# Kernel tuning notes

Hardware: AMD Instinct MI355X
Metric: run time of the kernel (lower is better)

## Reference

```python
import jax, jax.numpy as jnp
import numpy as np

N_NODES = 100000
N_EDGES = 3200000
C_FEAT = 512
F_OUT = 1


def setup_inputs() -> dict:
    key = jax.random.key(0)
    k1, k2, k3 = jax.random.split(key, 3)
    x = jax.random.normal(k1, (N_NODES, C_FEAT), dtype=jnp.float32)
    edge_index = jax.random.randint(k2, (2, N_EDGES), 0, N_NODES, dtype=jnp.int64)
    # GCNConv lin weight (glorot-ish scale) and zero-init bias, as in PyG defaults
    W = jax.random.normal(k3, (F_OUT, C_FEAT), dtype=jnp.float32) / np.sqrt(C_FEAT)
    b = jnp.zeros((F_OUT,), dtype=jnp.float32)
    return {"x": x, "edge_index": edge_index, "W": W, "b": b}


def reference(x, edge_index, W, b):
    N = x.shape[0]
    # GCNConv: project first (lin has no bias), then normalized aggregation
    h = x @ W.T  # [N, F_OUT]
    # add self-loops
    loops = jnp.arange(N, dtype=edge_index.dtype)
    row = jnp.concatenate([edge_index[0], loops])  # source
    col = jnp.concatenate([edge_index[1], loops])  # target
    # symmetric normalization: deg over targets (incl. self-loop weight 1)
    deg = jax.ops.segment_sum(jnp.ones_like(col, dtype=h.dtype), col, num_segments=N)
    dinv = jnp.where(deg > 0, jax.lax.rsqrt(deg), 0.0)
    norm = dinv[row] * dinv[col]  # [E+N]
    msg = h[row] * norm[:, None]  # gather + scale
    out = jax.ops.segment_sum(msg, col, num_segments=N) + b  # scatter-add + bias
    # F_out == 1 branch of forward
    return jax.nn.sigmoid(out)
```

## Files before the change

### kernel.cpp

```cpp
#include <hip/hip_runtime.h>
#include <hip/hip_fp16.h>
#include <math.h>

#define NN 100000
#define NE 3200000
#define CF 512

#define NPARTS  8
#define PART    12500
#define NSLICES 64
#define EPB     (NE / NSLICES)
#define NPB     (NSLICES * NPARTS)

#define OFF_H    12800000
#define OFF_G    13200000
#define OFF_DINV 13600000

__device__ __forceinline__ bool detect_f64(const int* __restrict__ e32) {
    unsigned v = ((const unsigned*)e32)[2 * (threadIdx.x & 63) + 1];
    return __ballot(v != 0u) == 0ULL;
}

__device__ __forceinline__ int4 load_col4(const int* __restrict__ e32, bool f64, int e) {
    if (f64) {
        const int4* q = (const int4*)(e32 + 2 * (NE + e));
        int4 a = q[0], b = q[1];
        return make_int4(a.x, a.z, b.x, b.z);
    }
    return *(const int4*)(e32 + NE + e);
}

__device__ __forceinline__ int4 load_row4(const int* __restrict__ e32, bool f64, int e) {
    if (f64) {
        const int4* q = (const int4*)(e32 + 2 * e);
        int4 a = q[0], b = q[1];
        return make_int4(a.x, a.z, b.x, b.z);
    }
    return *(const int4*)(e32 + e);
}

#define NODES_PER_BLK 196

__global__ __launch_bounds__(1024) void deg_h_kernel(const int* __restrict__ e32,
                                                     const float* __restrict__ x,
                                                     const float* __restrict__ W,
                                                     unsigned short* __restrict__ deg_part,
                                                     float* __restrict__ h) {
    __shared__ int hist[PART];
    int tid = threadIdx.x;
    for (int i = tid; i < PART; i += 1024) hist[i] = 0;
    __syncthreads();

    int w = tid >> 6, lane = tid & 63;
    if (w < 12) {
        bool f64 = detect_f64(e32);
        int p = blockIdx.x >> 6;
        int s = blockIdx.x & 63;
        int lo = p * PART;
        int base = s * EPB;
        for (int e = base + tid * 4; e < base + EPB; e += 3072) {
            int4 c = load_col4(e32, f64, e);
            unsigned l0 = (unsigned)(c.x - lo), l1 = (unsigned)(c.y - lo);
            unsigned l2 = (unsigned)(c.z - lo), l3 = (unsigned)(c.w - lo);
            if (l0 < PART) atomicAdd(&hist[l0], 1);
            if (l1 < PART) atomicAdd(&hist[l1], 1);
            if (l2 < PART) atomicAdd(&hist[l2], 1);
            if (l3 < PART) atomicAdd(&hist[l3], 1);
        }
    } else {
        const float4* Wr = (const float4*)W;
        float4 w0 = Wr[lane], w1 = Wr[lane + 64];
        int start = blockIdx.x * NODES_PER_BLK;
        int end = start + NODES_PER_BLK;
        for (int i = start + (w - 12) * 2; i < end; i += 8) {
            int i1 = i + 1;
            float s0 = 0.f, s1 = 0.f;
            if (i < NN) {
                const float4* xr = (const float4*)(x + (size_t)i * CF);
                float4 a = xr[lane], bq = xr[lane + 64];
                s0 = a.x * w0.x + a.y * w0.y + a.z * w0.z + a.w * w0.w
                   + bq.x * w1.x + bq.y * w1.y + bq.z * w1.z + bq.w * w1.w;
            }
            if (i1 < NN) {
                const float4* xr = (const float4*)(x + (size_t)i1 * CF);
                float4 a = xr[lane], bq = xr[lane + 64];
                s1 = a.x * w0.x + a.y * w0.y + a.z * w0.z + a.w * w0.w
                   + bq.x * w1.x + bq.y * w1.y + bq.z * w1.z + bq.w * w1.w;
            }
#pragma unroll
            for (int off = 32; off >= 1; off >>= 1) {
                s0 += __shfl_down(s0, off, 64);
                s1 += __shfl_down(s1, off, 64);
            }
            if (lane == 0) {
                if (i < NN) h[i] = s0;
                if (i1 < NN) h[i1] = s1;
            }
        }
    }
    __syncthreads();
    unsigned short* outp = deg_part + (size_t)blockIdx.x * PART;
    for (int i = tid; i < PART; i += 1024) outp[i] = (unsigned short)hist[i];
}

__global__ void dinv_g_kernel(const unsigned short* __restrict__ deg_part,
                              const float* __restrict__ h,
                              float* __restrict__ dinv,
                              float* __restrict__ g) {
    int i = blockIdx.x * blockDim.x + threadIdx.x;
    if (i >= NN) return;
    int p = i / PART, l = i - p * PART;
    const unsigned short* bp = deg_part + ((size_t)(p << 6)) * PART + l;
    int d = 1;
#pragma unroll
    for (int s = 0; s < NSLICES; ++s) d += bp[(size_t)s * PART];
    float di = rsqrtf((float)d);
    dinv[i] = di;
    g[i] = h[i] * di;
}

__global__ __launch_bounds__(1024) void scatter_lds_kernel(const int* __restrict__ e32,
                                                           const float* __restrict__ g,
                                                           __half* __restrict__ s_part) {
    __shared__ float hs[PART];
    int tid = threadIdx.x;
    for (int i = tid; i < PART; i += 1024) hs[i] = 0.f;
    __syncthreads();

    bool f64 = detect_f64(e32);
    int p = blockIdx.x >> 6;
    int s = blockIdx.x & 63;
    int lo = p * PART;
    int base = s * EPB;
    for (int e = base + tid * 4; e < base + EPB; e += 4096) {
        int4 c = load_col4(e32, f64, e);
        int4 r = load_row4(e32, f64, e);
        unsigned l0 = (unsigned)(c.x - lo), l1 = (unsigned)(c.y - lo);
        unsigned l2 = (unsigned)(c.z - lo), l3 = (unsigned)(c.w - lo);
        if (l0 < PART) atomicAdd(&hs[l0], g[r.x]);
        if (l1 < PART) atomicAdd(&hs[l1], g[r.y]);
        if (l2 < PART) atomicAdd(&hs[l2], g[r.z]);
        if (l3 < PART) atomicAdd(&hs[l3], g[r.w]);
    }
    __syncthreads();
    __half* outp = s_part + (size_t)blockIdx.x * PART;
    for (int i = tid; i < PART; i += 1024) outp[i] = __float2half(hs[i]);
}

__global__ void final_kernel(const __half* __restrict__ s_part,
                             const float* __restrict__ g,
                             const float* __restrict__ dinv,
                             const float* __restrict__ b,
                             float* __restrict__ out) {
    int i = blockIdx.x * blockDim.x + threadIdx.x;
    if (i >= NN) return;
    int p = i / PART, l = i - p * PART;
    const __half* bp = s_part + ((size_t)(p << 6)) * PART + l;
    float acc = g[i];
#pragma unroll
    for (int s = 0; s < NSLICES; ++s) acc += __half2float(bp[(size_t)s * PART]);
    float v = dinv[i] * acc + b[0];
    out[i] = 1.f / (1.f + expf(-v));
}

extern "C" void kernel_launch(void* const* d_in, const int* in_sizes, int n_in,
                              void* d_out, int out_size, void* d_ws, size_t ws_size,
                              hipStream_t stream) {
    const float* x = (const float*)d_in[0];
    const int* eidx = (const int*)d_in[1];
    const float* W = (const float*)d_in[2];
    const float* b = (const float*)d_in[3];
    float* out = (float*)d_out;

    char* ws = (char*)d_ws;
    unsigned short* part_u16 = (unsigned short*)(ws);
    __half* part_h = (__half*)(ws);
    float* h = (float*)(ws + OFF_H);
    float* g = (float*)(ws + OFF_G);
    float* dinv = (float*)(ws + OFF_DINV);

    deg_h_kernel<<<NPB, 1024, 0, stream>>>(eidx, x, W, part_u16, h);
    dinv_g_kernel<<<(NN + 255) / 256, 256, 0, stream>>>(part_u16, h, dinv, g);
    scatter_lds_kernel<<<NPB, 1024, 0, stream>>>(eidx, g, part_h);
    final_kernel<<<(NN + 255) / 256, 256, 0, stream>>>(part_h, g, dinv, b, out);
}
```

Before: 368.4 us.

## Replace partitioned LDS histograms with direct global atomics for degree and scatter

The per-partition shared-memory histograms with fp16/u16 partial buffers are dropped in favour of direct global atomicAdd into a single float sum array and a single uint degree array, cleared by a memset. This removes the 8x redundant edge scans, the partial-buffer writes and the 64-way reductions in the finalisation kernels. In exchange it relies on global atomic throughput and contention in L2 on MI355X, and the float atomic ordering becomes nondeterministic. The degree/projection kernel is also split into separate edge and projection blocks of 256 threads.

```diff
diff --git a/kernel.cpp b/kernel.cpp
--- a/kernel.cpp
+++ b/kernel.cpp
@@ -1,27 +1,22 @@
 #include <hip/hip_runtime.h>
-#include <hip/hip_fp16.h>
 #include <math.h>
 
 #define NN 100000
 #define NE 3200000
 #define CF 512
 
-#define NPARTS  8
-#define PART    12500
-#define NSLICES 64
-#define EPB     (NE / NSLICES)
-#define NPB     (NSLICES * NPARTS)
+#define OFF_S    0
+#define OFF_DEG  400000
+#define OFF_H    800000
+#define OFF_G    1200000
+#define OFF_DINV 1600000
 
-#define OFF_H    12800000
-#define OFF_G    13200000
-#define OFF_DINV 13600000
-
-__device__ __forceinline__ bool detect_f64(const int* __restrict__ e32) {
+__device__ __forceinline__ bool detect_f64(const int* e32) {
     unsigned v = ((const unsigned*)e32)[2 * (threadIdx.x & 63) + 1];
     return __ballot(v != 0u) == 0ULL;
 }
 
-__device__ __forceinline__ int4 load_col4(const int* __restrict__ e32, bool f64, int e) {
+__device__ __forceinline__ int4 load_col4(const int* e32, bool f64, int e) {
     if (f64) {
         const int4* q = (const int4*)(e32 + 2 * (NE + e));
         int4 a = q[0], b = q[1];
@@ -29,8 +24,7 @@
     }
     return *(const int4*)(e32 + NE + e);
 }
-
-__device__ __forceinline__ int4 load_row4(const int* __restrict__ e32, bool f64, int e) {
+__device__ __forceinline__ int4 load_row4(const int* e32, bool f64, int e) {
     if (f64) {
         const int4* q = (const int4*)(e32 + 2 * e);
         int4 a = q[0], b = q[1];
@@ -39,43 +33,37 @@
     return *(const int4*)(e32 + e);
 }
 
-#define NODES_PER_BLK 196
+#define EDGE_BLKS 512
+#define H_BLKS    1536
+#define K1_BLKS   (EDGE_BLKS + H_BLKS)
 
-__global__ __launch_bounds__(1024) void deg_h_kernel(const int* __restrict__ e32,
-                                                     const float* __restrict__ x,
-                                                     const float* __restrict__ W,
-                                                     unsigned short* __restrict__ deg_part,
-                                                     float* __restrict__ h) {
-    __shared__ int hist[PART];
-    int tid = threadIdx.x;
-    for (int i = tid; i < PART; i += 1024) hist[i] = 0;
-    __syncthreads();
-
-    int w = tid >> 6, lane = tid & 63;
-    if (w < 12) {
+__global__ __launch_bounds__(256) void deg_h_kernel(const int* __restrict__ e32,
+                                                    const float* __restrict__ x,
+                                                    const float* __restrict__ W,
+                                                    unsigned* __restrict__ deg,
+                                                    float* __restrict__ h) {
+    int blk = blockIdx.x;
+    if (blk < EDGE_BLKS) {
         bool f64 = detect_f64(e32);
-        int p = blockIdx.x >> 6;
-        int s = blockIdx.x & 63;
-        int lo = p * PART;
-        int base = s * EPB;
-        for (int e = base + tid * 4; e < base + EPB; e += 3072) {
+        int gid = blk * 256 + threadIdx.x;
+        const int STRIDE = EDGE_BLKS * 256 * 4;
+        for (int e = gid * 4; e < NE; e += STRIDE) {
             int4 c = load_col4(e32, f64, e);
-            unsigned l0 = (unsigned)(c.x - lo), l1 = (unsigned)(c.y - lo);
-            unsigned l2 = (unsigned)(c.z - lo), l3 = (unsigned)(c.w - lo);
-            if (l0 < PART) atomicAdd(&hist[l0], 1);
-            if (l1 < PART) atomicAdd(&hist[l1], 1);
-            if (l2 < PART) atomicAdd(&hist[l2], 1);
-            if (l3 < PART) atomicAdd(&hist[l3], 1);
+            atomicAdd(&deg[c.x], 1u);
+            atomicAdd(&deg[c.y], 1u);
+            atomicAdd(&deg[c.z], 1u);
+            atomicAdd(&deg[c.w], 1u);
         }
     } else {
+        int wave = (blk - EDGE_BLKS) * 4 + (threadIdx.x >> 6);
+        int lane = threadIdx.x & 63;
         const float4* Wr = (const float4*)W;
         float4 w0 = Wr[lane], w1 = Wr[lane + 64];
-        int start = blockIdx.x * NODES_PER_BLK;
-        int end = start + NODES_PER_BLK;
-        for (int i = start + (w - 12) * 2; i < end; i += 8) {
+        const int NWAVES = H_BLKS * 4;
+        for (int i = wave * 2; i < NN; i += NWAVES * 2) {
             int i1 = i + 1;
             float s0 = 0.f, s1 = 0.f;
-            if (i < NN) {
+            {
                 const float4* xr = (const float4*)(x + (size_t)i * CF);
                 float4 a = xr[lane], bq = xr[lane + 64];
                 s0 = a.x * w0.x + a.y * w0.y + a.z * w0.z + a.w * w0.w
@@ -93,73 +81,50 @@
                 s1 += __shfl_down(s1, off, 64);
             }
             if (lane == 0) {
-                if (i < NN) h[i] = s0;
+                h[i] = s0;
                 if (i1 < NN) h[i1] = s1;
             }
         }
     }
-    __syncthreads();
-    unsigned short* outp = deg_part + (size_t)blockIdx.x * PART;
-    for (int i = tid; i < PART; i += 1024) outp[i] = (unsigned short)hist[i];
 }
 
-__global__ void dinv_g_kernel(const unsigned short* __restrict__ deg_part,
-                              const float* __restrict__ h,
-                              float* __restrict__ dinv,
-                              float* __restrict__ g) {
-    int i = blockIdx.x * blockDim.x + threadIdx.x;
+__global__ __launch_bounds__(256) void dinv_g_kernel(const unsigned* __restrict__ deg,
+                                                     const float* __restrict__ h,
+                                                     float* __restrict__ dinv,
+                                                     float* __restrict__ g) {
+    int i = blockIdx.x * 256 + threadIdx.x;
     if (i >= NN) return;
-    int p = i / PART, l = i - p * PART;
-    const unsigned short* bp = deg_part + ((size_t)(p << 6)) * PART + l;
-    int d = 1;
-#pragma unroll
-    for (int s = 0; s < NSLICES; ++s) d += bp[(size_t)s * PART];
-    float di = rsqrtf((float)d);
+    float di = rsqrtf((float)(1u + deg[i]));
     dinv[i] = di;
     g[i] = h[i] * di;
 }
 
-__global__ __launch_bounds__(1024) void scatter_lds_kernel(const int* __restrict__ e32,
-                                                           const float* __restrict__ g,
-                                                           __half* __restrict__ s_part) {
-    __shared__ float hs[PART];
-    int tid = threadIdx.x;
-    for (int i = tid; i < PART; i += 1024) hs[i] = 0.f;
-    __syncthreads();
-
+#define SC_BLKS 1024
+__global__ __launch_bounds__(256) void scatter_kernel(const int* __restrict__ e32,
+                                                      const float* __restrict__ g,
+                                                      float* __restrict__ s) {
     bool f64 = detect_f64(e32);
-    int p = blockIdx.x >> 6;
-    int s = blockIdx.x & 63;
-    int lo = p * PART;
-    int base = s * EPB;
-    for (int e = base + tid * 4; e < base + EPB; e += 4096) {
+    int gid = blockIdx.x * 256 + threadIdx.x;
+    const int STRIDE = SC_BLKS * 256 * 4;
+    for (int e = gid * 4; e < NE; e += STRIDE) {
         int4 c = load_col4(e32, f64, e);
         int4 r = load_row4(e32, f64, e);
-        unsigned l0 = (unsigned)(c.x - lo), l1 = (unsigned)(c.y - lo);
-        unsigned l2 = (unsigned)(c.z - lo), l3 = (unsigned)(c.w - lo);
-        if (l0 < PART) atomicAdd(&hs[l0], g[r.x]);
-        if (l1 < PART) atomicAdd(&hs[l1], g[r.y]);
-        if (l2 < PART) atomicAdd(&hs[l2], g[r.z]);
-        if (l3 < PART) atomicAdd(&hs[l3], g[r.w]);
+        float g0 = g[r.x], g1 = g[r.y], g2 = g[r.z], g3 = g[r.w];
+        atomicAdd(&s[c.x], g0);
+        atomicAdd(&s[c.y], g1);
+        atomicAdd(&s[c.z], g2);
+        atomicAdd(&s[c.w], g3);
     }
-    __syncthreads();
-    __half* outp = s_part + (size_t)blockIdx.x * PART;
-    for (int i = tid; i < PART; i += 1024) outp[i] = __float2half(hs[i]);
 }
 
-__global__ void final_kernel(const __half* __restrict__ s_part,
-                             const float* __restrict__ g,
-                             const float* __restrict__ dinv,
-                             const float* __restrict__ b,
-                             float* __restrict__ out) {
-    int i = blockIdx.x * blockDim.x + threadIdx.x;
+__global__ __launch_bounds__(256) void final_kernel(const float* __restrict__ s,
+                                                    const float* __restrict__ g,
+                                                    const float* __restrict__ dinv,
+                                                    const float* __restrict__ b,
+                                                    float* __restrict__ out) {
+    int i = blockIdx.x * 256 + threadIdx.x;
     if (i >= NN) return;
-    int p = i / PART, l = i - p * PART;
-    const __half* bp = s_part + ((size_t)(p << 6)) * PART + l;
-    float acc = g[i];
-#pragma unroll
-    for (int s = 0; s < NSLICES; ++s) acc += __half2float(bp[(size_t)s * PART]);
-    float v = dinv[i] * acc + b[0];
+    float v = dinv[i] * (s[i] + g[i]) + b[0];
     out[i] = 1.f / (1.f + expf(-v));
 }
 
@@ -173,14 +138,16 @@
     float* out = (float*)d_out;
 
     char* ws = (char*)d_ws;
-    unsigned short* part_u16 = (unsigned short*)(ws);
-    __half* part_h = (__half*)(ws);
+    float* s = (float*)(ws + OFF_S);
+    unsigned* deg = (unsigned*)(ws + OFF_DEG);
     float* h = (float*)(ws + OFF_H);
     float* g = (float*)(ws + OFF_G);
     float* dinv = (float*)(ws + OFF_DINV);
 
-    deg_h_kernel<<<NPB, 1024, 0, stream>>>(eidx, x, W, part_u16, h);
-    dinv_g_kernel<<<(NN + 255) / 256, 256, 0, stream>>>(part_u16, h, dinv, g);
-    scatter_lds_kernel<<<NPB, 1024, 0, stream>>>(eidx, g, part_h);
-    final_kernel<<<(NN + 255) / 256, 256, 0, stream>>>(part_h, g, dinv, b, out);
+    hipMemsetAsync(ws, 0, 800000, stream);
+
+    deg_h_kernel<<<K1_BLKS, 256, 0, stream>>>(eidx, x, W, deg, h);
+    dinv_g_kernel<<<(NN + 255) / 256, 256, 0, stream>>>(deg, h, dinv, g);
+    scatter_kernel<<<SC_BLKS, 256, 0, stream>>>(eidx, g, s);
+    final_kernel<<<(NN + 255) / 256, 256, 0, stream>>>(s, g, dinv, b, out);
 }
```

After: 574.2 us. 55.8% more time.

## Fuse GCN pipeline into single cooperative kernel with grid syncs

Applied to the files above, without the earlier changes.

Replaces the four-kernel sequence (degree histogram plus projection, dinv/g, LDS scatter, final reduce) with one cooperative kernel. It uses grid.sync between phases and keeps h and dinv in LDS instead of global memory. The goal is to remove inter-kernel launch gaps and some global round trips. The trade-off is the cost of grid-wide barriers and a required co-residency of all 512 1024-thread blocks. If the cooperative launch fails, it falls back to the old kernels.

```diff
diff --git a/kernel.cpp b/kernel.cpp
--- a/kernel.cpp
+++ b/kernel.cpp
@@ -1,6 +1,9 @@
 #include <hip/hip_runtime.h>
 #include <hip/hip_fp16.h>
+#include <hip/hip_cooperative_groups.h>
 #include <math.h>
+
+namespace cg = cooperative_groups;
 
 #define NN 100000
 #define NE 3200000
@@ -11,17 +14,18 @@
 #define NSLICES 64
 #define EPB     (NE / NSLICES)
 #define NPB     (NSLICES * NPARTS)
-
-#define OFF_H    12800000
-#define OFF_G    13200000
+#define NODES_PER_BLK 196
+
+#define OFF_G    12800000
+#define OFF_H    13200000
 #define OFF_DINV 13600000
 
-__device__ __forceinline__ bool detect_f64(const int* __restrict__ e32) {
+__device__ __forceinline__ bool detect_f64(const int* e32) {
     unsigned v = ((const unsigned*)e32)[2 * (threadIdx.x & 63) + 1];
     return __ballot(v != 0u) == 0ULL;
 }
 
-__device__ __forceinline__ int4 load_col4(const int* __restrict__ e32, bool f64, int e) {
+__device__ __forceinline__ int4 load_col4(const int* e32, bool f64, int e) {
     if (f64) {
         const int4* q = (const int4*)(e32 + 2 * (NE + e));
         int4 a = q[0], b = q[1];
@@ -29,8 +33,7 @@
     }
     return *(const int4*)(e32 + NE + e);
 }
-
-__device__ __forceinline__ int4 load_row4(const int* __restrict__ e32, bool f64, int e) {
+__device__ __forceinline__ int4 load_row4(const int* e32, bool f64, int e) {
     if (f64) {
         const int4* q = (const int4*)(e32 + 2 * e);
         int4 a = q[0], b = q[1];
@@ -39,7 +42,119 @@
     return *(const int4*)(e32 + e);
 }
 
-#define NODES_PER_BLK 196
+__global__ __launch_bounds__(1024, 8) void gcn_fused(const int* e32, const float* x,
+                                                     const float* W, const float* bias,
+                                                     unsigned short* part_u16,
+                                                     __half* part_h,
+                                                     float* g, float* out) {
+    __shared__ int hist[PART];
+    __shared__ float h_lds[NODES_PER_BLK];
+    __shared__ float dinv_lds[NODES_PER_BLK];
+    cg::grid_group grid = cg::this_grid();
+
+    int tid = threadIdx.x;
+    int blk = blockIdx.x;
+    int w = tid >> 6, lane = tid & 63;
+    bool f64 = detect_f64(e32);
+    int p = blk >> 6, s = blk & 63;
+    int lo = p * PART, base = s * EPB;
+
+    for (int i = tid; i < PART; i += 1024) hist[i] = 0;
+    __syncthreads();
+    if (w < 12) {
+        for (int e = base + tid * 4; e < base + EPB; e += 3072) {
+            int4 c = load_col4(e32, f64, e);
+            unsigned l0 = (unsigned)(c.x - lo), l1 = (unsigned)(c.y - lo);
+            unsigned l2 = (unsigned)(c.z - lo), l3 = (unsigned)(c.w - lo);
+            if (l0 < PART) atomicAdd(&hist[l0], 1);
+            if (l1 < PART) atomicAdd(&hist[l1], 1);
+            if (l2 < PART) atomicAdd(&hist[l2], 1);
+            if (l3 < PART) atomicAdd(&hist[l3], 1);
+        }
+    } else {
+        const float4* Wr = (const float4*)W;
+        float4 w0 = Wr[lane], w1 = Wr[lane + 64];
+        int start = blk * NODES_PER_BLK;
+        int end = start + NODES_PER_BLK;
+        for (int i = start + (w - 12) * 2; i < end; i += 8) {
+            int i1 = i + 1;
+            float s0 = 0.f, s1 = 0.f;
+            if (i < NN) {
+                const float4* xr = (const float4*)(x + (size_t)i * CF);
+                float4 a = xr[lane], bq = xr[lane + 64];
+                s0 = a.x * w0.x + a.y * w0.y + a.z * w0.z + a.w * w0.w
+                   + bq.x * w1.x + bq.y * w1.y + bq.z * w1.z + bq.w * w1.w;
+            }
+            if (i1 < NN) {
+                const float4* xr = (const float4*)(x + (size_t)i1 * CF);
+                float4 a = xr[lane], bq = xr[lane + 64];
+                s1 = a.x * w0.x + a.y * w0.y + a.z * w0.z + a.w * w0.w
+                   + bq.x * w1.x + bq.y * w1.y + bq.z * w1.z + bq.w * w1.w;
+            }
+#pragma unroll
+            for (int off = 32; off >= 1; off >>= 1) {
+                s0 += __shfl_down(s0, off, 64);
+                s1 += __shfl_down(s1, off, 64);
+            }
+            if (lane == 0) {
+                h_lds[i - start] = s0;
+                h_lds[i1 - start] = s1;
+            }
+        }
+    }
+    __syncthreads();
+    {
+        unsigned short* outp = part_u16 + (size_t)blk * PART;
+        for (int i = tid; i < PART; i += 1024) outp[i] = (unsigned short)hist[i];
+    }
+    __threadfence();
+    grid.sync();
+
+    int node = blk * NODES_PER_BLK + tid;
+    if (tid < NODES_PER_BLK && node < NN) {
+        int pp = node / PART, l = node - pp * PART;
+        const unsigned short* bp = part_u16 + ((size_t)(pp << 6)) * PART + l;
+        int d = 1;
+#pragma unroll 16
+        for (int ss = 0; ss < NSLICES; ++ss) d += bp[(size_t)ss * PART];
+        float di = rsqrtf((float)d);
+        dinv_lds[tid] = di;
+        g[node] = h_lds[tid] * di;
+    }
+    __threadfence();
+    grid.sync();
+
+    float* histf = (float*)hist;
+    for (int i = tid; i < PART; i += 1024) histf[i] = 0.f;
+    __syncthreads();
+    for (int e = base + tid * 4; e < base + EPB; e += 4096) {
+        int4 c = load_col4(e32, f64, e);
+        int4 r = load_row4(e32, f64, e);
+        unsigned l0 = (unsigned)(c.x - lo), l1 = (unsigned)(c.y - lo);
+        unsigned l2 = (unsigned)(c.z - lo), l3 = (unsigned)(c.w - lo);
+        if (l0 < PART) atomicAdd(&histf[l0], g[r.x]);
+        if (l1 < PART) atomicAdd(&histf[l1], g[r.y]);
+        if (l2 < PART) atomicAdd(&histf[l2], g[r.z]);
+        if (l3 < PART) atomicAdd(&histf[l3], g[r.w]);
+    }
+    __syncthreads();
+    {
+        __half* outp = part_h + (size_t)blk * PART;
+        for (int i = tid; i < PART; i += 1024) outp[i] = __float2half(histf[i]);
+    }
+    __threadfence();
+    grid.sync();
+
+    if (tid < NODES_PER_BLK && node < NN) {
+        int pp = node / PART, l = node - pp * PART;
+        const __half* bp = part_h + ((size_t)(pp << 6)) * PART + l;
+        float acc = g[node];
+#pragma unroll 16
+        for (int ss = 0; ss < NSLICES; ++ss) acc += __half2float(bp[(size_t)ss * PART]);
+        float v = dinv_lds[tid] * acc + bias[0];
+        out[node] = 1.f / (1.f + expf(-v));
+    }
+}
 
 __global__ __launch_bounds__(1024) void deg_h_kernel(const int* __restrict__ e32,
                                                      const float* __restrict__ x,
@@ -50,7 +165,6 @@
     int tid = threadIdx.x;
     for (int i = tid; i < PART; i += 1024) hist[i] = 0;
     __syncthreads();
-
     int w = tid >> 6, lane = tid & 63;
     if (w < 12) {
         bool f64 = detect_f64(e32);
@@ -126,7 +240,6 @@
     int tid = threadIdx.x;
     for (int i = tid; i < PART; i += 1024) hs[i] = 0.f;
     __syncthreads();
-
     bool f64 = detect_f64(e32);
     int p = blockIdx.x >> 6;
     int s = blockIdx.x & 63;
@@ -175,12 +288,19 @@
     char* ws = (char*)d_ws;
     unsigned short* part_u16 = (unsigned short*)(ws);
     __half* part_h = (__half*)(ws);
+    float* g = (float*)(ws + OFF_G);
     float* h = (float*)(ws + OFF_H);
-    float* g = (float*)(ws + OFF_G);
     float* dinv = (float*)(ws + OFF_DINV);
 
-    deg_h_kernel<<<NPB, 1024, 0, stream>>>(eidx, x, W, part_u16, h);
-    dinv_g_kernel<<<(NN + 255) / 256, 256, 0, stream>>>(part_u16, h, dinv, g);
-    scatter_lds_kernel<<<NPB, 1024, 0, stream>>>(eidx, g, part_h);
-    final_kernel<<<(NN + 255) / 256, 256, 0, stream>>>(part_h, g, dinv, b, out);
-}
+    void* kargs[] = {(void*)&eidx, (void*)&x, (void*)&W, (void*)&b,
+                     (void*)&part_u16, (void*)&part_h, (void*)&g, (void*)&out};
+    hipError_t err = hipLaunchCooperativeKernel((const void*)gcn_fused,
+                                                dim3(NPB), dim3(1024),
+                                                kargs, 0, stream);
+    if (err != hipSuccess) {
+        deg_h_kernel<<<NPB, 1024, 0, stream>>>(eidx, x, W, part_u16, h);
+        dinv_g_kernel<<<(NN + 255) / 256, 256, 0, stream>>>(part_u16, h, dinv, g);
+        scatter_lds_kernel<<<NPB, 1024, 0, stream>>>(eidx, g, part_h);
+        final_kernel<<<(NN + 255) / 256, 256, 0, stream>>>(part_h, g, dinv, b, out);
+    }
+}
```

Result: slower. 1.117 ms (+203.1%).

## Fuse final reduction into scatter kernel via last-block counter, halve slices

Applied to the files above, without the earlier changes.

Merges the final per-node reduction and sigmoid into the scatter kernel: each partition's last-arriving block, found through an atomic counter, sums the fp16 partials and writes the output. It also halves the number of edge slices per partition to 32, giving 256 blocks instead of 512, so there are fewer partials to reduce. The gathers of g are hoisted ahead of the LDS atomics so the loads can overlap. The aim is to drop one kernel launch and cut partial-sum traffic, at the cost of fewer blocks to fill the GPU and a serial tail in one block per partition.

```diff
diff --git a/kernel.cpp b/kernel.cpp
--- a/kernel.cpp
+++ b/kernel.cpp
@@ -11,17 +11,24 @@
 #define NSLICES 64
 #define EPB     (NE / NSLICES)
 #define NPB     (NSLICES * NPARTS)
-
-#define OFF_H    12800000
-#define OFF_G    13200000
-#define OFF_DINV 13600000
-
-__device__ __forceinline__ bool detect_f64(const int* __restrict__ e32) {
+#define NODES_PER_BLK 196
+
+#define SNSL    32
+#define SEPB    (NE / SNSL)
+#define SNPB    (SNSL * NPARTS)
+
+#define OFF_SPART 12800000
+#define OFF_G     19200000
+#define OFF_H     19600000
+#define OFF_DINV  20000000
+#define OFF_CTR   20400000
+
+__device__ __forceinline__ bool detect_f64(const int* e32) {
     unsigned v = ((const unsigned*)e32)[2 * (threadIdx.x & 63) + 1];
     return __ballot(v != 0u) == 0ULL;
 }
 
-__device__ __forceinline__ int4 load_col4(const int* __restrict__ e32, bool f64, int e) {
+__device__ __forceinline__ int4 load_col4(const int* e32, bool f64, int e) {
     if (f64) {
         const int4* q = (const int4*)(e32 + 2 * (NE + e));
         int4 a = q[0], b = q[1];
@@ -29,8 +36,7 @@
     }
     return *(const int4*)(e32 + NE + e);
 }
-
-__device__ __forceinline__ int4 load_row4(const int* __restrict__ e32, bool f64, int e) {
+__device__ __forceinline__ int4 load_row4(const int* e32, bool f64, int e) {
     if (f64) {
         const int4* q = (const int4*)(e32 + 2 * e);
         int4 a = q[0], b = q[1];
@@ -39,18 +45,17 @@
     return *(const int4*)(e32 + e);
 }
 
-#define NODES_PER_BLK 196
-
 __global__ __launch_bounds__(1024) void deg_h_kernel(const int* __restrict__ e32,
                                                      const float* __restrict__ x,
                                                      const float* __restrict__ W,
                                                      unsigned short* __restrict__ deg_part,
-                                                     float* __restrict__ h) {
+                                                     float* __restrict__ h,
+                                                     unsigned* __restrict__ ctr) {
     __shared__ int hist[PART];
     int tid = threadIdx.x;
+    if (blockIdx.x == 0 && tid < 8) ctr[tid] = 0u;
     for (int i = tid; i < PART; i += 1024) hist[i] = 0;
     __syncthreads();
-
     int w = tid >> 6, lane = tid & 63;
     if (w < 12) {
         bool f64 = detect_f64(e32);
@@ -119,48 +124,61 @@
     g[i] = h[i] * di;
 }
 
-__global__ __launch_bounds__(1024) void scatter_lds_kernel(const int* __restrict__ e32,
-                                                           const float* __restrict__ g,
-                                                           __half* __restrict__ s_part) {
+__global__ __launch_bounds__(1024) void scatter_final(const int* __restrict__ e32,
+                                                      const float* __restrict__ g,
+                                                      const float* __restrict__ dinv,
+                                                      const float* __restrict__ b,
+                                                      __half* __restrict__ spart,
+                                                      unsigned* __restrict__ ctr,
+                                                      float* __restrict__ out) {
     __shared__ float hs[PART];
+    __shared__ int lastflag;
     int tid = threadIdx.x;
     for (int i = tid; i < PART; i += 1024) hs[i] = 0.f;
     __syncthreads();
 
     bool f64 = detect_f64(e32);
-    int p = blockIdx.x >> 6;
-    int s = blockIdx.x & 63;
+    int p = blockIdx.x >> 5;
+    int s = blockIdx.x & 31;
     int lo = p * PART;
-    int base = s * EPB;
-    for (int e = base + tid * 4; e < base + EPB; e += 4096) {
+    int base = s * SEPB;
+    for (int e = base + tid * 4; e < base + SEPB; e += 4096) {
         int4 c = load_col4(e32, f64, e);
         int4 r = load_row4(e32, f64, e);
+        float g0 = g[r.x], g1 = g[r.y], g2 = g[r.z], g3 = g[r.w];
         unsigned l0 = (unsigned)(c.x - lo), l1 = (unsigned)(c.y - lo);
         unsigned l2 = (unsigned)(c.z - lo), l3 = (unsigned)(c.w - lo);
-        if (l0 < PART) atomicAdd(&hs[l0], g[r.x]);
-        if (l1 < PART) atomicAdd(&hs[l1], g[r.y]);
-        if (l2 < PART) atomicAdd(&hs[l2], g[r.z]);
-        if (l3 < PART) atomicAdd(&hs[l3], g[r.w]);
-    }
-    __syncthreads();
-    __half* outp = s_part + (size_t)blockIdx.x * PART;
-    for (int i = tid; i < PART; i += 1024) outp[i] = __float2half(hs[i]);
-}
-
-__global__ void final_kernel(const __half* __restrict__ s_part,
-                             const float* __restrict__ g,
-                             const float* __restrict__ dinv,
-                             const float* __restrict__ b,
-                             float* __restrict__ out) {
-    int i = blockIdx.x * blockDim.x + threadIdx.x;
-    if (i >= NN) return;
-    int p = i / PART, l = i - p * PART;
-    const __half* bp = s_part + ((size_t)(p << 6)) * PART + l;
-    float acc = g[i];
-#pragma unroll
-    for (int s = 0; s < NSLICES; ++s) acc += __half2float(bp[(size_t)s * PART]);
-    float v = dinv[i] * acc + b[0];
-    out[i] = 1.f / (1.f + expf(-v));
+        if (l0 < PART) atomicAdd(&hs[l0], g0);
+        if (l1 < PART) atomicAdd(&hs[l1], g1);
+        if (l2 < PART) atomicAdd(&hs[l2], g2);
+        if (l3 < PART) atomicAdd(&hs[l3], g3);
+    }
+    __syncthreads();
+    {
+        __half* outp = spart + (size_t)blockIdx.x * PART;
+        for (int i = tid; i < PART; i += 1024) outp[i] = __float2half(hs[i]);
+    }
+
+    __threadfence();
+    __syncthreads();
+    if (tid == 0) {
+        unsigned old = atomicAdd(&ctr[p], 1u);
+        lastflag = (old == (unsigned)(SNSL - 1)) ? 1 : 0;
+    }
+    __syncthreads();
+    if (!lastflag) return;
+    __threadfence();
+
+    const __half* bp = spart + (size_t)(p * SNSL) * PART;
+    float bias = b[0];
+    for (int l = tid; l < PART; l += 1024) {
+        float acc = 0.f;
+#pragma unroll 8
+        for (int s2 = 0; s2 < SNSL; ++s2) acc += __half2float(bp[(size_t)s2 * PART + l]);
+        int i = lo + l;
+        float v = dinv[i] * (acc + g[i]) + bias;
+        out[i] = 1.f / (1.f + expf(-v));
+    }
 }
 
 extern "C" void kernel_launch(void* const* d_in, const int* in_sizes, int n_in,
@@ -173,14 +191,14 @@
     float* out = (float*)d_out;
 
     char* ws = (char*)d_ws;
-    unsigned short* part_u16 = (unsigned short*)(ws);
-    __half* part_h = (__half*)(ws);
+    unsigned short* dpart = (unsigned short*)(ws);
+    __half* spart = (__half*)(ws + OFF_SPART);
+    float* g = (float*)(ws + OFF_G);
     float* h = (float*)(ws + OFF_H);
-    float* g = (float*)(ws + OFF_G);
     float* dinv = (float*)(ws + OFF_DINV);
-
-    deg_h_kernel<<<NPB, 1024, 0, stream>>>(eidx, x, W, part_u16, h);
-    dinv_g_kernel<<<(NN + 255) / 256, 256, 0, stream>>>(part_u16, h, dinv, g);
-    scatter_lds_kernel<<<NPB, 1024, 0, stream>>>(eidx, g, part_h);
-    final_kernel<<<(NN + 255) / 256, 256, 0, stream>>>(part_h, g, dinv, b, out);
-}
+    unsigned* ctr = (unsigned*)(ws + OFF_CTR);
+
+    deg_h_kernel<<<NPB, 1024, 0, stream>>>(eidx, x, W, dpart, h, ctr);
+    dinv_g_kernel<<<(NN + 255) / 256, 256, 0, stream>>>(dpart, h, dinv, g);
+    scatter_final<<<SNPB, 1024, 0, stream>>>(eidx, g, dinv, b, spart, ctr, out);
+}
```

Measured after the change: 553.9 us. +50.3%, slower.
